# Performance work log

Measured on AMD Instinct MI355X. Metric: run time of the kernel, lower is better.

## Reference

```python
import jax, jax.numpy as jnp
import numpy as np

N = 8192
H = 512

def setup_inputs() -> dict:
    key = jax.random.key(0)
    ks = jax.random.split(key, 11)
    s = 1.0 / np.sqrt(H)
    return {
        "q": jax.random.normal(ks[0], (N, H), dtype=jnp.float32),
        "k": jax.random.normal(ks[1], (N, H), dtype=jnp.float32),
        "v": jax.random.normal(ks[2], (N, H), dtype=jnp.float32),
        "Wq": jax.random.uniform(ks[3], (H, H), jnp.float32, -s, s),
        "bq": jax.random.uniform(ks[4], (H,), jnp.float32, -s, s),
        "Wk": jax.random.uniform(ks[5], (H, H), jnp.float32, -s, s),
        "bk": jax.random.uniform(ks[6], (H,), jnp.float32, -s, s),
        "Wv": jax.random.uniform(ks[7], (H, H), jnp.float32, -s, s),
        "bv": jax.random.uniform(ks[8], (H,), jnp.float32, -s, s),
        "Wo": jax.random.uniform(ks[9], (H, H), jnp.float32, -s, s),
        "bo": jax.random.uniform(ks[10], (H,), jnp.float32, -s, s),
    }

def reference(q, k, v, Wq, bq, Wk, bk, Wv, bv, Wo, bo):
    # torch Linear: x @ W.T + b
    qp = q @ Wq.T + bq            # [N, H]
    kp = k @ Wk.T + bk            # [N, H]
    vp = v @ Wv.T + bv            # [N, H]
    weights = qp @ kp.T           # [N, N]  (no 1/sqrt(d) scaling in original)
    normalized = jax.nn.softmax(weights, axis=-1)  # [N, N]
    out = normalized @ vp         # [N, H]
    out = out @ Wo.T + bo         # [N, H]
    return (out, normalized)
```

## Files before the change

### kernel.cpp

```cpp
#include <hip/hip_runtime.h>

typedef unsigned short u16;
typedef _Float16 f16x8 __attribute__((ext_vector_type(8)));
typedef u16 u16x8 __attribute__((ext_vector_type(8)));
typedef float floatx4 __attribute__((ext_vector_type(4)));

#define DEV __device__ __forceinline__

DEV u16 f2h(float f) {
  _Float16 h = (_Float16)f;
  return __builtin_bit_cast(u16, h);
}

typedef __attribute__((address_space(3))) void lds_void_t;
typedef const __attribute__((address_space(1))) void gbl_void_t;

DEV void async16(const void* g, void* l) {
  __builtin_amdgcn_global_load_lds((gbl_void_t*)g, (lds_void_t*)l, 16, 0, 0);
}


__global__ __launch_bounds__(256) void k_cvt16(const float* __restrict__ x,
                                               u16* __restrict__ o, int n4) {
  int i = blockIdx.x * 256 + threadIdx.x;
  if (i >= n4) return;
  float4 v = ((const float4*)x)[i];
  *(ushort4*)&o[4 * (size_t)i] =
      make_ushort4(f2h(v.x), f2h(v.y), f2h(v.z), f2h(v.w));
}


__global__ __launch_bounds__(256) void k_transpose(const u16* __restrict__ in,
                                                   u16* __restrict__ out,
                                                   int R, int C) {
  __shared__ u16 T[64][72];
  int m0 = blockIdx.x * 64;
  int n0 = blockIdx.y * 64;
  int t = threadIdx.x;
#pragma unroll
  for (int i = 0; i < 2; ++i) {
    int lin = i * 2048 + t * 8;
    int r = lin >> 6, c = lin & 63;
    u16x8 d = *(const u16x8*)&in[(size_t)(m0 + r) * C + n0 + c];
#pragma unroll
    for (int j = 0; j < 8; ++j) T[r][c + j] = d[j];
  }
  __syncthreads();
#pragma unroll
  for (int i = 0; i < 2; ++i) {
    int lin = i * 2048 + t * 8;
    int r = lin >> 6, c = lin & 63;
    u16x8 d;
#pragma unroll
    for (int j = 0; j < 8; ++j) d[j] = T[c + j][r];
    *(u16x8*)&out[(size_t)(n0 + r) * R + m0 + c] = d;
  }
}


template <bool WRITEP>
__global__ __launch_bounds__(256) void k_softmax(float* __restrict__ W,
                                                 u16* __restrict__ P) {
  const size_t row = blockIdx.x;
  float4* pv = (float4*)(W + row * 8192);
  const int t = threadIdx.x;
  const int w = t >> 6, l = t & 63;
  float4 v[8];
#pragma unroll
  for (int i = 0; i < 8; ++i) v[i] = pv[i * 256 + t];
  float m = -1e30f;
#pragma unroll
  for (int i = 0; i < 8; ++i)
    m = fmaxf(m, fmaxf(fmaxf(v[i].x, v[i].y), fmaxf(v[i].z, v[i].w)));
#pragma unroll
  for (int o = 32; o >= 1; o >>= 1) m = fmaxf(m, __shfl_xor(m, o, 64));
  __shared__ float redm[4];
  __shared__ float reds[4];
  if (l == 0) redm[w] = m;
  __syncthreads();
  m = fmaxf(fmaxf(redm[0], redm[1]), fmaxf(redm[2], redm[3]));
  float s = 0.f;
#pragma unroll
  for (int i = 0; i < 8; ++i) {
    v[i].x = __expf(v[i].x - m); s += v[i].x;
    v[i].y = __expf(v[i].y - m); s += v[i].y;
    v[i].z = __expf(v[i].z - m); s += v[i].z;
    v[i].w = __expf(v[i].w - m); s += v[i].w;
  }
#pragma unroll
  for (int o = 32; o >= 1; o >>= 1) s += __shfl_xor(s, o, 64);
  if (l == 0) reds[w] = s;
  __syncthreads();
  s = (reds[0] + reds[1]) + (reds[2] + reds[3]);
  float inv = 1.0f / s;
#pragma unroll
  for (int i = 0; i < 8; ++i) {
    v[i].x *= inv; v[i].y *= inv; v[i].z *= inv; v[i].w *= inv;
    pv[i * 256 + t] = v[i];
    if constexpr (WRITEP) {
      *(ushort4*)&P[row * 8192 + (size_t)(i * 256 + t) * 4] =
          make_ushort4(f2h(v[i].x), f2h(v[i].y), f2h(v[i].z), f2h(v[i].w));
    }
  }
}


template <int BN, bool AF32, int OMODE, bool BIAS>
__global__ __launch_bounds__(256, 2)
void k_gemm(const void* A_, const u16* __restrict__ Bh,
            const float* __restrict__ bias, void* C_, int K, int lda, int ldb,
            int ldc) {
  constexpr int NT = BN / 32;
  constexpr int BCHW = BN / 64;
  __shared__ alignas(16) u16 Ash[128 * 32];
  __shared__ alignas(16) u16 Bsh[BN * 32];

  const int m0 = blockIdx.x * 128;
  const int n0 = blockIdx.y * BN;
  const int tid = threadIdx.x;
  const int w = tid >> 6;
  const int l = tid & 63;
  const int lr = l & 15;
  const int lq = l >> 4;
  const int wr = (w >> 1) * 64;
  const int wc = (w & 1) * (BN / 2);
  const int srow = l >> 2;
  const int scol = (l & 3) * 8;

  const u16* Ah = (const u16*)A_;
  const float* Af = (const float*)A_;

  floatx4 acc[4][NT] = {};

  for (int k0 = 0; k0 < K; k0 += 32) {
    __syncthreads();
    if constexpr (!AF32) {
#pragma unroll
      for (int i = 0; i < 2; ++i) {
        int c = w * 2 + i;
        int row = c * 16 + srow;
        async16(Ah + (size_t)(m0 + row) * lda + k0 + scol, &Ash[c * 512]);
      }
    } else {
#pragma unroll
      for (int i = 0; i < 2; ++i) {
        int lin = i * 2048 + tid * 8;
        int row = lin >> 5, col = lin & 31;
        const float* g = Af + (size_t)(m0 + row) * lda + k0 + col;
        float4 u0 = *(const float4*)g;
        float4 u1 = *(const float4*)(g + 4);
        u16x8 tv;
        tv[0] = f2h(u0.x); tv[1] = f2h(u0.y); tv[2] = f2h(u0.z); tv[3] = f2h(u0.w);
        tv[4] = f2h(u1.x); tv[5] = f2h(u1.y); tv[6] = f2h(u1.z); tv[7] = f2h(u1.w);
        *(u16x8*)&Ash[lin] = tv;
      }
    }
#pragma unroll
    for (int i = 0; i < BCHW; ++i) {
      int c = w * BCHW + i;
      int row = c * 16 + srow;
      async16(Bh + (size_t)(n0 + row) * ldb + k0 + scol, &Bsh[c * 512]);
    }
    __syncthreads();

    f16x8 fa[4], fb[NT];
#pragma unroll
    for (int t = 0; t < 4; ++t)
      fa[t] = *(const f16x8*)&Ash[(wr + t * 16 + lr) * 32 + lq * 8];
#pragma unroll
    for (int t = 0; t < NT; ++t)
      fb[t] = *(const f16x8*)&Bsh[(wc + t * 16 + lr) * 32 + lq * 8];
#pragma unroll
    for (int mt = 0; mt < 4; ++mt)
#pragma unroll
      for (int nt = 0; nt < NT; ++nt)
        acc[mt][nt] = __builtin_amdgcn_mfma_f32_16x16x32_f16(
            fa[mt], fb[nt], acc[mt][nt], 0, 0, 0);
  }

  float bv[NT];
#pragma unroll
  for (int nt = 0; nt < NT; ++nt)
    bv[nt] = BIAS ? bias[n0 + wc + nt * 16 + lr] : 0.f;
#pragma unroll
  for (int mt = 0; mt < 4; ++mt)
#pragma unroll
    for (int nt = 0; nt < NT; ++nt)
#pragma unroll
      for (int r = 0; r < 4; ++r) {
        float x = acc[mt][nt][r] + bv[nt];
        int row = m0 + wr + mt * 16 + lq * 4 + r;
        int col = n0 + wc + nt * 16 + lr;
        size_t idx = (size_t)row * ldc + col;
        if constexpr (OMODE == 0) {
          ((float*)C_)[idx] = x;
        } else {
          ((u16*)C_)[idx] = f2h(x);
        }
      }
}


extern "C" void kernel_launch(void* const* d_in, const int* in_sizes, int n_in,
                              void* d_out, int out_size, void* d_ws,
                              size_t ws_size, hipStream_t stream) {
  constexpr int N = 8192, H = 512;
  const float* q   = (const float*)d_in[0];
  const float* kin = (const float*)d_in[1];
  const float* v   = (const float*)d_in[2];
  const float* Wq  = (const float*)d_in[3];
  const float* bq  = (const float*)d_in[4];
  const float* Wk  = (const float*)d_in[5];
  const float* bk  = (const float*)d_in[6];
  const float* Wv  = (const float*)d_in[7];
  const float* bv  = (const float*)d_in[8];
  const float* Wo  = (const float*)d_in[9];
  const float* bo  = (const float*)d_in[10];
  float* out  = (float*)d_out;
  float* norm = out + (size_t)N * H;

  char* ws = (char*)d_ws;
  const size_t MB = 1024 * 1024;
  u16* xh   = (u16*)(ws + 0 * MB);
  u16* wb   = (u16*)(ws + 8 * MB);
  u16* qp   = (u16*)(ws + 9 * MB);
  u16* kp   = (u16*)(ws + 17 * MB);
  u16* vp   = (u16*)(ws + 25 * MB);
  u16* vpT  = (u16*)(ws + 33 * MB);
  u16* Pf   = (u16*)(ws + 41 * MB);
  u16* out0 = vp;

  const bool usePf = ws_size >= 41 * MB + (size_t)N * N * 2;

  dim3 blk(256);

  k_cvt16<<<4096, blk, 0, stream>>>(q, xh, (N * H) / 4);
  k_cvt16<<<256, blk, 0, stream>>>(Wq, wb, (H * H) / 4);
  k_gemm<64, false, 1, true><<<dim3(64, 8), blk, 0, stream>>>(
      xh, wb, bq, qp, H, H, H, H);

  k_cvt16<<<4096, blk, 0, stream>>>(kin, xh, (N * H) / 4);
  k_cvt16<<<256, blk, 0, stream>>>(Wk, wb, (H * H) / 4);
  k_gemm<64, false, 1, true><<<dim3(64, 8), blk, 0, stream>>>(
      xh, wb, bk, kp, H, H, H, H);

  k_cvt16<<<4096, blk, 0, stream>>>(v, xh, (N * H) / 4);
  k_cvt16<<<256, blk, 0, stream>>>(Wv, wb, (H * H) / 4);
  k_gemm<64, false, 1, true><<<dim3(64, 8), blk, 0, stream>>>(
      xh, wb, bv, vp, H, H, H, H);
  k_transpose<<<dim3(128, 8), blk, 0, stream>>>(vp, vpT, N, H);

  k_gemm<128, false, 0, false><<<dim3(64, 64), blk, 0, stream>>>(
      qp, kp, nullptr, norm, H, H, H, N);

  if (usePf)
    k_softmax<true><<<N, blk, 0, stream>>>(norm, Pf);
  else
    k_softmax<false><<<N, blk, 0, stream>>>(norm, nullptr);

  if (usePf)
    k_gemm<64, false, 1, false><<<dim3(64, 8), blk, 0, stream>>>(
        Pf, vpT, nullptr, out0, N, N, N, H);
  else
    k_gemm<64, true, 1, false><<<dim3(64, 8), blk, 0, stream>>>(
        norm, vpT, nullptr, out0, N, N, N, H);

  k_cvt16<<<256, blk, 0, stream>>>(Wo, wb, (H * H) / 4);
  k_gemm<64, false, 0, true><<<dim3(64, 8), blk, 0, stream>>>(
      out0, wb, bo, out, H, H, H, H);
}
```

Measured before the change: 730.1 us.

## Multi-stage async LDS prefetch pipeline in fp16 GEMM with vmcnt waits

Replaces the single-buffered load-then-compute loop in the f16-input GEMM with a ring of D+1 LDS buffers (D=3 or 4 stages in flight). It uses explicit s_waitcnt vmcnt counts plus one barrier per iteration, so global-to-LDS loads overlap with MFMA work. The goal is to hide global memory latency that previously stalled each K step. In exchange it uses several times more LDS per block, which may lower occupancy. It also relies on the vmcnt literals matching the exact number of loads issued per stage, and clamps out-of-range prefetches to the last tile.

```diff
diff --git a/kernel.cpp b/kernel.cpp
--- a/kernel.cpp
+++ b/kernel.cpp
@@ -17,6 +17,17 @@
 
 DEV void async16(const void* g, void* l) {
   __builtin_amdgcn_global_load_lds((gbl_void_t*)g, (lds_void_t*)l, 16, 0, 0);
+}
+
+template <int N>
+DEV void wait_vm() {
+  static_assert(N == 0 || N == 6 || N == 8 || N == 9 || N == 12,
+                "add vmcnt literal");
+  if constexpr (N == 0) asm volatile("s_waitcnt vmcnt(0)" ::: "memory");
+  else if constexpr (N == 6) asm volatile("s_waitcnt vmcnt(6)" ::: "memory");
+  else if constexpr (N == 8) asm volatile("s_waitcnt vmcnt(8)" ::: "memory");
+  else if constexpr (N == 9) asm volatile("s_waitcnt vmcnt(9)" ::: "memory");
+  else if constexpr (N == 12) asm volatile("s_waitcnt vmcnt(12)" ::: "memory");
 }
 
 
@@ -112,8 +123,11 @@
             int ldc) {
   constexpr int NT = BN / 32;
   constexpr int BCHW = BN / 64;
-  __shared__ alignas(16) u16 Ash[128 * 32];
-  __shared__ alignas(16) u16 Bsh[BN * 32];
+  constexpr int D = (BN == 128) ? 3 : 4;
+  constexpr int BC = AF32 ? 1 : (D + 1);
+  constexpr int LPI = 2 + BCHW;
+  __shared__ alignas(16) u16 Ash[BC][128 * 32];
+  __shared__ alignas(16) u16 Bsh[BC][BN * 32];
 
   const int m0 = blockIdx.x * 128;
   const int n0 = blockIdx.y * BN;
@@ -132,16 +146,54 @@
 
   floatx4 acc[4][NT] = {};
 
-  for (int k0 = 0; k0 < K; k0 += 32) {
-    __syncthreads();
-    if constexpr (!AF32) {
+  if constexpr (!AF32) {
+    const int nIter = K / 32;
+    auto STAGE = [&](int t, int b) {
+      const int k0 = (t < nIter ? t : nIter - 1) * 32;
 #pragma unroll
       for (int i = 0; i < 2; ++i) {
         int c = w * 2 + i;
         int row = c * 16 + srow;
-        async16(Ah + (size_t)(m0 + row) * lda + k0 + scol, &Ash[c * 512]);
-      }
-    } else {
+        async16(Ah + (size_t)(m0 + row) * lda + k0 + scol, &Ash[b][c * 512]);
+      }
+#pragma unroll
+      for (int i = 0; i < BCHW; ++i) {
+        int c = w * BCHW + i;
+        int row = c * 16 + srow;
+        async16(Bh + (size_t)(n0 + row) * ldb + k0 + scol, &Bsh[b][c * 512]);
+      }
+    };
+
+#pragma unroll
+    for (int t = 0; t < D; ++t) STAGE(t, t);
+
+    int bcon = 0;
+    int bpro = D % BC;
+    for (int t = 0; t < nIter; ++t) {
+      wait_vm<LPI * (D - 1)>();
+      __builtin_amdgcn_s_barrier();
+      STAGE(t + D, bpro);
+
+      f16x8 fa[4], fb[NT];
+#pragma unroll
+      for (int x = 0; x < 4; ++x)
+        fa[x] = *(const f16x8*)&Ash[bcon][(wr + x * 16 + lr) * 32 + lq * 8];
+#pragma unroll
+      for (int x = 0; x < NT; ++x)
+        fb[x] = *(const f16x8*)&Bsh[bcon][(wc + x * 16 + lr) * 32 + lq * 8];
+#pragma unroll
+      for (int mt = 0; mt < 4; ++mt)
+#pragma unroll
+        for (int nt = 0; nt < NT; ++nt)
+          acc[mt][nt] = __builtin_amdgcn_mfma_f32_16x16x32_f16(
+              fa[mt], fb[nt], acc[mt][nt], 0, 0, 0);
+
+      if (++bcon == BC) bcon = 0;
+      if (++bpro == BC) bpro = 0;
+    }
+  } else {
+    for (int k0 = 0; k0 < K; k0 += 32) {
+      __syncthreads();
 #pragma unroll
       for (int i = 0; i < 2; ++i) {
         int lin = i * 2048 + tid * 8;
@@ -152,30 +204,30 @@
         u16x8 tv;
         tv[0] = f2h(u0.x); tv[1] = f2h(u0.y); tv[2] = f2h(u0.z); tv[3] = f2h(u0.w);
         tv[4] = f2h(u1.x); tv[5] = f2h(u1.y); tv[6] = f2h(u1.z); tv[7] = f2h(u1.w);
-        *(u16x8*)&Ash[lin] = tv;
-      }
+        *(u16x8*)&Ash[0][lin] = tv;
+      }
+#pragma unroll
+      for (int i = 0; i < BCHW; ++i) {
+        int c = w * BCHW + i;
+        int row = c * 16 + srow;
+        async16(Bh + (size_t)(n0 + row) * ldb + k0 + scol, &Bsh[0][c * 512]);
+      }
+      __syncthreads();
+
+      f16x8 fa[4], fb[NT];
+#pragma unroll
+      for (int t = 0; t < 4; ++t)
+        fa[t] = *(const f16x8*)&Ash[0][(wr + t * 16 + lr) * 32 + lq * 8];
+#pragma unroll
+      for (int t = 0; t < NT; ++t)
+        fb[t] = *(const f16x8*)&Bsh[0][(wc + t * 16 + lr) * 32 + lq * 8];
+#pragma unroll
+      for (int mt = 0; mt < 4; ++mt)
+#pragma unroll
+        for (int nt = 0; nt < NT; ++nt)
+          acc[mt][nt] = __builtin_amdgcn_mfma_f32_16x16x32_f16(
+              fa[mt], fb[nt], acc[mt][nt], 0, 0, 0);
     }
-#pragma unroll
-    for (int i = 0; i < BCHW; ++i) {
-      int c = w * BCHW + i;
-      int row = c * 16 + srow;
-      async16(Bh + (size_t)(n0 + row) * ldb + k0 + scol, &Bsh[c * 512]);
-    }
-    __syncthreads();
-
-    f16x8 fa[4], fb[NT];
-#pragma unroll
-    for (int t = 0; t < 4; ++t)
-      fa[t] = *(const f16x8*)&Ash[(wr + t * 16 + lr) * 32 + lq * 8];
-#pragma unroll
-    for (int t = 0; t < NT; ++t)
-      fb[t] = *(const f16x8*)&Bsh[(wc + t * 16 + lr) * 32 + lq * 8];
-#pragma unroll
-    for (int mt = 0; mt < 4; ++mt)
-#pragma unroll
-      for (int nt = 0; nt < NT; ++nt)
-        acc[mt][nt] = __builtin_amdgcn_mfma_f32_16x16x32_f16(
-            fa[mt], fb[nt], acc[mt][nt], 0, 0, 0);
   }
 
   float bv[NT];
```

Result: slower. 757.0 us (+3.7%).
